# Kernel tuning notes

Hardware: AMD Instinct MI355X
Metric: run time of the kernel (lower is better)

The kernel has to match this reference:

```python
import jax, jax.numpy as jnp
import numpy as np

N_TOKENS, MODEL_DIM, NUM_EXPERTS = 65536, 1024, 64
CAPACITY_FACTOR = 1.0


def setup_inputs() -> dict:
    key = jax.random.key(0)
    k1, k2 = jax.random.split(key)
    x = jax.random.normal(k1, (N_TOKENS, MODEL_DIM), dtype=jnp.float32)
    # gate projection weight, torch Linear stores [out_features, in_features]
    wg = jax.random.normal(k2, (NUM_EXPERTS, MODEL_DIM), dtype=jnp.float32) * (1.0 / np.sqrt(MODEL_DIM))
    return {"x": x, "wg": wg}


def reference(x, wg):
    N, E = x.shape[0], wg.shape[0]
    logits = x @ wg.T                              # [N, E]
    # training-branch capacity: capacity_factor * ceil(N / E)
    capacity = int(CAPACITY_FACTOR * ((N + E - 1) // E))
    indices1_s = jnp.argmax(logits, axis=1)        # [N] top-1 expert per token
    gates = jax.nn.softmax(logits, axis=1)         # [N, E]
    mask1 = jax.nn.one_hot(indices1_s, E, dtype=gates.dtype)  # [N, E]
    gates1_s = jnp.sum(gates * mask1, axis=1)      # [N] gate value of chosen expert
    # locations1_s[i] = number of earlier tokens routed to the same expert
    # (exclusive prefix count = inclusive cumsum - 1 at the selected column)
    locations1 = jnp.cumsum(mask1, axis=0) - 1.0   # [N, E]
    locations1_s = jnp.sum(locations1 * mask1, axis=1).astype(jnp.int32)
    # auxiliary load-balance loss (float32 branch of the original)
    me = jnp.sum(gates, axis=0)                    # [E]
    ce = jnp.sum(mask1, axis=0)                    # [E]
    l_aux = jnp.sum(me * ce) * (E / (N * N))
    return (l_aux, indices1_s.astype(jnp.int32), capacity, locations1_s, gates1_s, E)
```

## Files before the change

kernel.cpp:

```cpp
#include <hip/hip_runtime.h>

#define NT 65536
#define MD 1024
#define NE 64
#define BK 32
#define NBLK (NT / 64)

__global__ __launch_bounds__(256) void gate_kernel(
    const float* __restrict__ x, const float* __restrict__ wg,
    float* __restrict__ out, unsigned* __restrict__ packed_ws,
    int* __restrict__ hist_ws, float* __restrict__ me)
{
    __shared__ __align__(16) float smem[4 * BK * 68];
    float (*as)[BK][68] = (float (*)[BK][68])smem;
    float (*bs)[BK][68] = (float (*)[BK][68])(smem + 2 * BK * 68);

    const int tid = threadIdx.x;
    const int tx = tid & 15;
    const int ty = tid >> 4;
    const int t0 = blockIdx.x * 64;

    const int r0 = tid >> 3, q0 = tid & 7;
    const int r1 = r0 + 32,  q1 = q0;
    const float* xa0 = x  + (size_t)(t0 + r0) * MD + q0 * 4;
    const float* xa1 = x  + (size_t)(t0 + r1) * MD + q1 * 4;
    const float* wa0 = wg + (size_t)r0 * MD + q0 * 4;
    const float* wa1 = wg + (size_t)r1 * MD + q1 * 4;

    float4 va0 = *(const float4*)(xa0);
    float4 va1 = *(const float4*)(xa1);
    float4 vw0 = *(const float4*)(wa0);
    float4 vw1 = *(const float4*)(wa1);

#define STAGE(buf)                                                      \
    do {                                                                \
        as[buf][q0 * 4 + 0][r0] = va0.x; as[buf][q0 * 4 + 1][r0] = va0.y; \
        as[buf][q0 * 4 + 2][r0] = va0.z; as[buf][q0 * 4 + 3][r0] = va0.w; \
        as[buf][q1 * 4 + 0][r1] = va1.x; as[buf][q1 * 4 + 1][r1] = va1.y; \
        as[buf][q1 * 4 + 2][r1] = va1.z; as[buf][q1 * 4 + 3][r1] = va1.w; \
        bs[buf][q0 * 4 + 0][r0] = vw0.x; bs[buf][q0 * 4 + 1][r0] = vw0.y; \
        bs[buf][q0 * 4 + 2][r0] = vw0.z; bs[buf][q0 * 4 + 3][r0] = vw0.w; \
        bs[buf][q1 * 4 + 0][r1] = vw1.x; bs[buf][q1 * 4 + 1][r1] = vw1.y; \
        bs[buf][q1 * 4 + 2][r1] = vw1.z; bs[buf][q1 * 4 + 3][r1] = vw1.w; \
    } while (0)

    STAGE(0);
    __syncthreads();

    float acc[4][4];
#pragma unroll
    for (int i = 0; i < 4; ++i)
#pragma unroll
        for (int j = 0; j < 4; ++j) acc[i][j] = 0.f;

    for (int it = 0; it < MD / BK; ++it) {
        const int cur = it & 1;
        if (it < MD / BK - 1) {
            const int kn = (it + 1) * BK;
            va0 = *(const float4*)(xa0 + kn);
            va1 = *(const float4*)(xa1 + kn);
            vw0 = *(const float4*)(wa0 + kn);
            vw1 = *(const float4*)(wa1 + kn);
        }
#pragma unroll
        for (int k = 0; k < BK; ++k) {
            float4 a = *(const float4*)&as[cur][k][ty * 4];
            float4 b = *(const float4*)&bs[cur][k][tx * 4];
            float av[4] = {a.x, a.y, a.z, a.w};
            float bv[4] = {b.x, b.y, b.z, b.w};
#pragma unroll
            for (int i = 0; i < 4; ++i)
#pragma unroll
                for (int j = 0; j < 4; ++j) acc[i][j] += av[i] * bv[j];
        }
        if (it < MD / BK - 1) {
            const int nb = cur ^ 1;
            STAGE(nb);
        }
        __syncthreads();
    }

    float* lt  = smem;
    float* inv = smem + 4160;

#pragma unroll
    for (int i = 0; i < 4; ++i)
#pragma unroll
        for (int j = 0; j < 4; ++j)
            lt[(ty * 4 + i) * 65 + tx * 4 + j] = acc[i][j];
    __syncthreads();

    if (tid < 64) {
        const int t = tid;
        float m = -1e30f; int am = 0;
        for (int e = 0; e < NE; ++e) {
            float v = lt[t * 65 + e];
            if (v > m) { m = v; am = e; }
        }
        float s = 0.f;
        for (int e = 0; e < NE; ++e) {
            float ev = __expf(lt[t * 65 + e] - m);
            lt[t * 65 + e] = ev;
            s += ev;
        }
        float g = 1.0f / s;
        const int gt = t0 + t;
        out[1 + gt] = (float)am;
        out[2 + 2 * NT + gt] = g;
        inv[t] = g;

        const unsigned long long below = (1ull << t) - 1ull;
        int rank = 0, mycnt = 0;
        for (int e = 0; e < NE; ++e) {
            unsigned long long msk = __ballot(am == e);
            if (t == e)  mycnt = (int)__popcll(msk);
            if (am == e) rank  = (int)__popcll(msk & below);
        }
        packed_ws[gt] = (unsigned)am | ((unsigned)rank << 8);
        hist_ws[blockIdx.x * NE + t] = mycnt;
    }
    __syncthreads();

    if (tid < NE) {
        const int e = tid;
        float s = 0.f;
        for (int t = 0; t < 64; ++t) s += lt[t * 65 + e] * inv[t];
        atomicAdd(&me[e], s);
    }
}

__global__ __launch_bounds__(256) void scan_kernel(
    int* __restrict__ hist_ws, float* __restrict__ ce)
{
    const int e = blockIdx.x;
    const int tid = threadIdx.x;
    const int lane = tid & 63, wave = tid >> 6;
    __shared__ int wtot[4];

    int h[4];
#pragma unroll
    for (int j = 0; j < 4; ++j) h[j] = hist_ws[(tid * 4 + j) * NE + e];
    int s = h[0] + h[1] + h[2] + h[3];

    int scan = s;
#pragma unroll
    for (int d = 1; d < 64; d <<= 1) {
        int o = __shfl_up(scan, d, 64);
        if (lane >= d) scan += o;
    }
    if (lane == 63) wtot[wave] = scan;
    __syncthreads();
    int wpre = 0;
#pragma unroll
    for (int w = 0; w < 4; ++w)
        if (w < wave) wpre += wtot[w];

    int run = wpre + scan - s;
#pragma unroll
    for (int j = 0; j < 4; ++j) {
        hist_ws[(tid * 4 + j) * NE + e] = run;
        run += h[j];
    }
    if (tid == 255) ce[e] = (float)run;
}

__global__ __launch_bounds__(256) void emit_kernel(
    const unsigned* __restrict__ packed_ws, const int* __restrict__ offs_ws,
    float* __restrict__ out)
{
    const int i = blockIdx.x * 256 + threadIdx.x;
    const unsigned p = packed_ws[i];
    const int am = (int)(p & 63u);
    const int rank = (int)(p >> 8);
    const int b = i >> 6;
    out[2 + NT + i] = (float)(offs_ws[b * NE + am] + rank);
}

__global__ void finalize_kernel(const float* __restrict__ me,
                                const float* __restrict__ ce,
                                float* __restrict__ out)
{
    int tid = threadIdx.x;
    float v = me[tid] * ce[tid];
#pragma unroll
    for (int d = 32; d > 0; d >>= 1) v += __shfl_down(v, d, 64);
    if (tid == 0) {
        out[0] = v * (float)((double)NE / ((double)NT * (double)NT));
        out[1 + NT] = 1024.0f;
        out[2 + 3 * NT] = 64.0f;
    }
}

extern "C" void kernel_launch(void* const* d_in, const int* in_sizes, int n_in,
                              void* d_out, int out_size, void* d_ws, size_t ws_size,
                              hipStream_t stream)
{
    const float* x  = (const float*)d_in[0];
    const float* wg = (const float*)d_in[1];
    float* out = (float*)d_out;

    unsigned* packed_ws = (unsigned*)d_ws;
    int* hist_ws = (int*)((char*)d_ws + (size_t)NT * 4);
    float* me = (float*)((char*)d_ws + (size_t)NT * 4 + (size_t)NBLK * NE * 4);
    float* ce = me + NE;

    hipMemsetAsync(me, 0, NE * sizeof(float), stream);
    gate_kernel<<<NBLK, 256, 0, stream>>>(x, wg, out, packed_ws, hist_ws, me);
    scan_kernel<<<NE, 256, 0, stream>>>(hist_ws, ce);
    emit_kernel<<<NT / 256, 256, 0, stream>>>(packed_ws, hist_ws, out);
    finalize_kernel<<<1, 64, 0, stream>>>(me, ce, out);
}
```

Baseline: 408.8 us.

## Store gate GEMM tiles row-major with XOR swizzle and vector LDS writes

Replaces the transposed, padded shared-memory tiles (16 scalar stores per thread per stage) with row-major tiles written as float4 and XOR-swizzled by row, so staging takes four vector stores. The inner loop now reads four float4 rows of A and B per 4-wide k step. Launch bounds are raised to request 4 blocks per CU. The intent is to cut LDS store instructions and bank conflicts; the risk is more LDS reads per FMA in the inner loop and register pressure from the occupancy hint.

Measured after the change: 424.3 us. 3.8% more time.

```diff
diff --git a/kernel.cpp b/kernel.cpp
--- a/kernel.cpp
+++ b/kernel.cpp
@@ -6,45 +6,41 @@
 #define BK 32
 #define NBLK (NT / 64)
 
-__global__ __launch_bounds__(256) void gate_kernel(
+#define SWZ(r, q) (((q) ^ (((r) >> 2) & 7)))
+
+__global__ __launch_bounds__(256, 4) void gate_kernel(
     const float* __restrict__ x, const float* __restrict__ wg,
     float* __restrict__ out, unsigned* __restrict__ packed_ws,
     int* __restrict__ hist_ws, float* __restrict__ me)
 {
-    __shared__ __align__(16) float smem[4 * BK * 68];
-    float (*as)[BK][68] = (float (*)[BK][68])smem;
-    float (*bs)[BK][68] = (float (*)[BK][68])(smem + 2 * BK * 68);
+    __shared__ __align__(16) float smem[2][128][32];
 
     const int tid = threadIdx.x;
     const int tx = tid & 15;
     const int ty = tid >> 4;
     const int t0 = blockIdx.x * 64;
 
-    const int r0 = tid >> 3, q0 = tid & 7;
-    const int r1 = r0 + 32,  q1 = q0;
-    const float* xa0 = x  + (size_t)(t0 + r0) * MD + q0 * 4;
-    const float* xa1 = x  + (size_t)(t0 + r1) * MD + q1 * 4;
-    const float* wa0 = wg + (size_t)r0 * MD + q0 * 4;
-    const float* wa1 = wg + (size_t)r1 * MD + q1 * 4;
-
-    float4 va0 = *(const float4*)(xa0);
-    float4 va1 = *(const float4*)(xa1);
-    float4 vw0 = *(const float4*)(wa0);
-    float4 vw1 = *(const float4*)(wa1);
-
-#define STAGE(buf)                                                      \
-    do {                                                                \
-        as[buf][q0 * 4 + 0][r0] = va0.x; as[buf][q0 * 4 + 1][r0] = va0.y; \
-        as[buf][q0 * 4 + 2][r0] = va0.z; as[buf][q0 * 4 + 3][r0] = va0.w; \
-        as[buf][q1 * 4 + 0][r1] = va1.x; as[buf][q1 * 4 + 1][r1] = va1.y; \
-        as[buf][q1 * 4 + 2][r1] = va1.z; as[buf][q1 * 4 + 3][r1] = va1.w; \
-        bs[buf][q0 * 4 + 0][r0] = vw0.x; bs[buf][q0 * 4 + 1][r0] = vw0.y; \
-        bs[buf][q0 * 4 + 2][r0] = vw0.z; bs[buf][q0 * 4 + 3][r0] = vw0.w; \
-        bs[buf][q1 * 4 + 0][r1] = vw1.x; bs[buf][q1 * 4 + 1][r1] = vw1.y; \
-        bs[buf][q1 * 4 + 2][r1] = vw1.z; bs[buf][q1 * 4 + 3][r1] = vw1.w; \
+    const int sr = tid >> 3;
+    const int sq = tid & 7;
+    const float* px0 = x  + (size_t)(t0 + sr) * MD + sq * 4;
+    const float* px1 = px0 + (size_t)32 * MD;
+    const float* pw0 = wg + (size_t)sr * MD + sq * 4;
+    const float* pw1 = pw0 + (size_t)32 * MD;
+
+    float4 g0 = *(const float4*)px0;
+    float4 g1 = *(const float4*)px1;
+    float4 g2 = *(const float4*)pw0;
+    float4 g3 = *(const float4*)pw1;
+
+#define STG(buf)                                                         \
+    do {                                                                 \
+        *(float4*)&smem[buf][sr      ][SWZ(sr,      sq) * 4] = g0;       \
+        *(float4*)&smem[buf][sr + 32 ][SWZ(sr + 32, sq) * 4] = g1;       \
+        *(float4*)&smem[buf][sr + 64 ][SWZ(sr + 64, sq) * 4] = g2;       \
+        *(float4*)&smem[buf][sr + 96 ][SWZ(sr + 96, sq) * 4] = g3;       \
     } while (0)
 
-    STAGE(0);
+    STG(0);
     __syncthreads();
 
     float acc[4][4];
@@ -57,31 +53,36 @@
         const int cur = it & 1;
         if (it < MD / BK - 1) {
             const int kn = (it + 1) * BK;
-            va0 = *(const float4*)(xa0 + kn);
-            va1 = *(const float4*)(xa1 + kn);
-            vw0 = *(const float4*)(wa0 + kn);
-            vw1 = *(const float4*)(wa1 + kn);
-        }
-#pragma unroll
-        for (int k = 0; k < BK; ++k) {
-            float4 a = *(const float4*)&as[cur][k][ty * 4];
-            float4 b = *(const float4*)&bs[cur][k][tx * 4];
-            float av[4] = {a.x, a.y, a.z, a.w};
-            float bv[4] = {b.x, b.y, b.z, b.w};
+            g0 = *(const float4*)(px0 + kn);
+            g1 = *(const float4*)(px1 + kn);
+            g2 = *(const float4*)(pw0 + kn);
+            g3 = *(const float4*)(pw1 + kn);
+        }
+#pragma unroll
+        for (int q = 0; q < 8; ++q) {
+            float4 A[4], B[4];
 #pragma unroll
             for (int i = 0; i < 4; ++i)
-#pragma unroll
-                for (int j = 0; j < 4; ++j) acc[i][j] += av[i] * bv[j];
-        }
-        if (it < MD / BK - 1) {
-            const int nb = cur ^ 1;
-            STAGE(nb);
-        }
+                A[i] = *(const float4*)&smem[cur][ty * 4 + i][SWZ(ty * 4 + i, q) * 4];
+#pragma unroll
+            for (int j = 0; j < 4; ++j)
+                B[j] = *(const float4*)&smem[cur][64 + tx * 4 + j][SWZ(64 + tx * 4 + j, q) * 4];
+#pragma unroll
+            for (int i = 0; i < 4; ++i)
+#pragma unroll
+                for (int j = 0; j < 4; ++j) {
+                    acc[i][j] = fmaf(A[i].x, B[j].x, acc[i][j]);
+                    acc[i][j] = fmaf(A[i].y, B[j].y, acc[i][j]);
+                    acc[i][j] = fmaf(A[i].z, B[j].z, acc[i][j]);
+                    acc[i][j] = fmaf(A[i].w, B[j].w, acc[i][j]);
+                }
+        }
+        if (it < MD / BK - 1) STG(cur ^ 1);
         __syncthreads();
     }
 
-    float* lt  = smem;
-    float* inv = smem + 4160;
+    float* lt  = &smem[0][0][0];
+    float* inv = lt + 4160;
 
 #pragma unroll
     for (int i = 0; i < 4; ++i)
```
